# Optimization experiments

Hardware: AMD Instinct MI355X
Metric: run time of the kernel (lower is better)

The kernel has to match this reference:

```python
import jax, jax.numpy as jnp
import numpy as np

PAD_IDX = 0
NEG_INF = -1e30

N_USERS, N_ITEMS, N_SUBJECTS, EMB_DIM = 100000, 100000, 10000, 16
B, L = 16384, 50


def setup_inputs() -> dict:
    key = jax.random.key(0)
    ks = jax.random.split(key, 10)
    subj_emb = jax.random.normal(ks[0], (N_SUBJECTS, EMB_DIM), dtype=jnp.float32) * 0.1
    subj_emb = subj_emb.at[PAD_IDX].set(0.0)  # padding_idx row is zeros in torch
    attn_w = jax.random.normal(ks[1], (EMB_DIM,), dtype=jnp.float32) * 0.25
    attn_b = jnp.zeros((), dtype=jnp.float32)
    user_bias = jax.random.normal(ks[2], (N_USERS,), dtype=jnp.float32) * 0.05
    item_bias = jax.random.normal(ks[3], (N_ITEMS,), dtype=jnp.float32) * 0.05
    global_bias = jnp.zeros((), dtype=jnp.float32)
    user_idx = jax.random.randint(ks[4], (B,), 0, N_USERS)
    item_idx = jax.random.randint(ks[5], (B,), 0, N_ITEMS)
    fav_subjects = jax.random.randint(ks[6], (B, L), 0, N_SUBJECTS)
    book_subjects = jax.random.randint(ks[7], (B, L), 0, N_SUBJECTS)
    return {
        "subj_emb": subj_emb, "attn_w": attn_w, "attn_b": attn_b,
        "user_bias": user_bias, "item_bias": item_bias, "global_bias": global_bias,
        "user_idx": user_idx, "item_idx": item_idx,
        "fav_subjects": fav_subjects, "book_subjects": book_subjects,
    }


def attention_pool(indices, subj_emb, attn_w, attn_b):
    embs = subj_emb[indices]                      # [B, L, D] gather
    scores = embs @ attn_w + attn_b               # [B, L] tiny linear (D->1)
    mask = indices != PAD_IDX                     # [B, L]
    has_real = jnp.any(mask, axis=1)              # [B]
    # rows with no real subjects get position 0 unmasked (torch per-row loop)
    safe_mask = mask.at[:, 0].set(mask[:, 0] | ~has_real)
    scores = jnp.where(safe_mask, scores, NEG_INF)
    weights = jax.nn.softmax(scores, axis=1)      # [B, L]
    pooled = jnp.einsum("bld,bl->bd", embs, weights)
    return pooled  # dropout is identity in eval mode


def reference(subj_emb, attn_w, attn_b, user_bias, item_bias, global_bias,
              user_idx, item_idx, fav_subjects, book_subjects):
    u_emb = attention_pool(fav_subjects, subj_emb, attn_w, attn_b)   # [B, D]
    i_emb = attention_pool(book_subjects, subj_emb, attn_w, attn_b)  # [B, D]
    dot = jnp.sum(u_emb * i_emb, axis=1)                             # [B]
    return dot + user_bias[user_idx] + item_bias[item_idx] + global_bias
```

## Files before the change

### kernel.cpp

```cpp
#include <hip/hip_runtime.h>
#include <math.h>


#define PAD_IDX 0
constexpr int D = 16;
constexpr int ROWS_PER_BLOCK = 8;
constexpr int THREADS = 256;

template <int LFIX>
__global__ __launch_bounds__(256) void pool_kernel(
    const float* __restrict__ subj_emb,
    const float* __restrict__ attn_w,
    const float* __restrict__ attn_b,
    const float* __restrict__ user_bias,
    const float* __restrict__ item_bias,
    const float* __restrict__ global_bias,
    const int*  __restrict__ user_idx,
    const int*  __restrict__ item_idx,
    const int*  __restrict__ fav_subjects,
    const int*  __restrict__ book_subjects,
    float* __restrict__ out,
    int B)
{
    __shared__ int sidx[2][ROWS_PER_BLOCK * LFIX];

    const int row0  = blockIdx.x * ROWS_PER_BLOCK;
    const int nInts = ROWS_PER_BLOCK * LFIX;
    const long base = (long)row0 * LFIX;

    {
        const int n4 = nInts >> 2;
        const int4* fsrc = (const int4*)(fav_subjects  + base);
        const int4* bsrc = (const int4*)(book_subjects + base);
        int4* fdst = (int4*)sidx[0];
        int4* bdst = (int4*)sidx[1];
        for (int i = threadIdx.x; i < n4; i += THREADS) {
            fdst[i] = fsrc[i];
            bdst[i] = bsrc[i];
        }
        for (int i = (n4 << 2) + threadIdx.x; i < nInts; i += THREADS) {
            sidx[0][i] = fav_subjects[base + i];
            sidx[1][i] = book_subjects[base + i];
        }
    }
    __syncthreads();

    const int t    = threadIdx.x;
    const int r    = t >> 5;
    const int c    = (t >> 3) & 3;
    const int pool = (t >> 2) & 1;
    const int j    = t & 3;
    const int row  = row0 + r;

    const float4 wv = *(const float4*)(attn_w + 4 * j);
    const float  bb = attn_b[0];

    const int* __restrict__ idxl = sidx[pool] + r * LFIX;

    float4 acc = {0.f, 0.f, 0.f, 0.f};
    float  s   = 0.f;

    constexpr int ITERS = (LFIX + 3) / 4;
    #pragma unroll
    for (int k = 0; k < ITERS; ++k) {
        const int l  = c + 4 * k;
        const int si = (l < LFIX) ? idxl[l] : PAD_IDX;
        const float4 e = *(const float4*)(subj_emb + (long)si * D + 4 * j);
        float p = e.x * wv.x + e.y * wv.y + e.z * wv.z + e.w * wv.w;
        p += __shfl_xor(p, 1, 4);
        p += __shfl_xor(p, 2, 4);
        const float ew = __expf(p + bb);
        const float w  = (si != PAD_IDX) ? ew : 0.f;
        s     += w;
        acc.x += w * e.x;
        acc.y += w * e.y;
        acc.z += w * e.z;
        acc.w += w * e.w;
    }

    acc.x += __shfl_xor(acc.x, 8, 32);  acc.x += __shfl_xor(acc.x, 16, 32);
    acc.y += __shfl_xor(acc.y, 8, 32);  acc.y += __shfl_xor(acc.y, 16, 32);
    acc.z += __shfl_xor(acc.z, 8, 32);  acc.z += __shfl_xor(acc.z, 16, 32);
    acc.w += __shfl_xor(acc.w, 8, 32);  acc.w += __shfl_xor(acc.w, 16, 32);
    s     += __shfl_xor(s,     8, 32);  s     += __shfl_xor(s,     16, 32);

    const float inv = (s > 0.f) ? (1.f / s) : 0.f;
    float4 u;
    u.x = acc.x * inv; u.y = acc.y * inv; u.z = acc.z * inv; u.w = acc.w * inv;

    float4 o;
    o.x = __shfl_xor(u.x, 4, 8);
    o.y = __shfl_xor(u.y, 4, 8);
    o.z = __shfl_xor(u.z, 4, 8);
    o.w = __shfl_xor(u.w, 4, 8);

    float prod = u.x * o.x + u.y * o.y + u.z * o.z + u.w * o.w;
    prod += __shfl_xor(prod, 1, 4);
    prod += __shfl_xor(prod, 2, 4);

    if (row < B && (t & 31) == 0) {
        out[row] = prod + user_bias[user_idx[row]]
                        + item_bias[item_idx[row]]
                        + global_bias[0];
    }
}

__global__ __launch_bounds__(256) void pool_kernel_gen(
    const float* __restrict__ subj_emb,
    const float* __restrict__ attn_w,
    const float* __restrict__ attn_b,
    const float* __restrict__ user_bias,
    const float* __restrict__ item_bias,
    const float* __restrict__ global_bias,
    const int*  __restrict__ user_idx,
    const int*  __restrict__ item_idx,
    const int*  __restrict__ fav_subjects,
    const int*  __restrict__ book_subjects,
    float* __restrict__ out,
    int B, int L)
{
    __shared__ int sidx[2][ROWS_PER_BLOCK * 128];
    const int row0  = blockIdx.x * ROWS_PER_BLOCK;
    const int nInts = ROWS_PER_BLOCK * L;
    const long base = (long)row0 * L;
    for (int i = threadIdx.x; i < nInts; i += THREADS) {
        sidx[0][i] = fav_subjects[base + i];
        sidx[1][i] = book_subjects[base + i];
    }
    __syncthreads();

    const int t    = threadIdx.x;
    const int r    = t >> 5;
    const int c    = (t >> 3) & 3;
    const int pool = (t >> 2) & 1;
    const int j    = t & 3;
    const int row  = row0 + r;
    const float4 wv = *(const float4*)(attn_w + 4 * j);
    const float  bb = attn_b[0];
    const int* __restrict__ idxl = sidx[pool] + r * L;

    float4 acc = {0.f, 0.f, 0.f, 0.f};
    float  s   = 0.f;
    for (int l = c; l < L; l += 4) {
        const int si = idxl[l];
        const float4 e = *(const float4*)(subj_emb + (long)si * D + 4 * j);
        float p = e.x * wv.x + e.y * wv.y + e.z * wv.z + e.w * wv.w;
        p += __shfl_xor(p, 1, 4);
        p += __shfl_xor(p, 2, 4);
        const float ew = __expf(p + bb);
        const float w  = (si != PAD_IDX) ? ew : 0.f;
        s += w;
        acc.x += w * e.x; acc.y += w * e.y; acc.z += w * e.z; acc.w += w * e.w;
    }
    acc.x += __shfl_xor(acc.x, 8, 32);  acc.x += __shfl_xor(acc.x, 16, 32);
    acc.y += __shfl_xor(acc.y, 8, 32);  acc.y += __shfl_xor(acc.y, 16, 32);
    acc.z += __shfl_xor(acc.z, 8, 32);  acc.z += __shfl_xor(acc.z, 16, 32);
    acc.w += __shfl_xor(acc.w, 8, 32);  acc.w += __shfl_xor(acc.w, 16, 32);
    s     += __shfl_xor(s,     8, 32);  s     += __shfl_xor(s,     16, 32);
    const float inv = (s > 0.f) ? (1.f / s) : 0.f;
    float4 u = {acc.x * inv, acc.y * inv, acc.z * inv, acc.w * inv};
    float4 o;
    o.x = __shfl_xor(u.x, 4, 8); o.y = __shfl_xor(u.y, 4, 8);
    o.z = __shfl_xor(u.z, 4, 8); o.w = __shfl_xor(u.w, 4, 8);
    float prod = u.x * o.x + u.y * o.y + u.z * o.z + u.w * o.w;
    prod += __shfl_xor(prod, 1, 4);
    prod += __shfl_xor(prod, 2, 4);
    if (row < B && (t & 31) == 0) {
        out[row] = prod + user_bias[user_idx[row]]
                        + item_bias[item_idx[row]] + global_bias[0];
    }
}

extern "C" void kernel_launch(void* const* d_in, const int* in_sizes, int n_in,
                              void* d_out, int out_size, void* d_ws, size_t ws_size,
                              hipStream_t stream) {
    const float* subj_emb    = (const float*)d_in[0];
    const float* attn_w      = (const float*)d_in[1];
    const float* attn_b      = (const float*)d_in[2];
    const float* user_bias   = (const float*)d_in[3];
    const float* item_bias   = (const float*)d_in[4];
    const float* global_bias = (const float*)d_in[5];
    const int*   user_idx    = (const int*)d_in[6];
    const int*   item_idx    = (const int*)d_in[7];
    const int*   fav_subj    = (const int*)d_in[8];
    const int*   book_subj   = (const int*)d_in[9];
    float*       out         = (float*)d_out;

    const int D_ = 16;
    const int B  = in_sizes[6];
    const int L  = in_sizes[8] / B;
    (void)D_; (void)d_ws; (void)ws_size;

    const int blocks = (B + ROWS_PER_BLOCK - 1) / ROWS_PER_BLOCK;
    if (L == 50) {
        pool_kernel<50><<<blocks, THREADS, 0, stream>>>(
            subj_emb, attn_w, attn_b, user_bias, item_bias, global_bias,
            user_idx, item_idx, fav_subj, book_subj, out, B);
    } else {
        pool_kernel_gen<<<blocks, THREADS, 0, stream>>>(
            subj_emb, attn_w, attn_b, user_bias, item_bias, global_bias,
            user_idx, item_idx, fav_subj, book_subj, out, B, L);
    }
}
```

Measured before the change: 85.39 us.

## Use one wavefront per row and batch embedding gathers ahead of compute

Rows per block drop from 8 to 4, so each 64-lane wavefront handles one batch row with 8 positions in flight instead of 4. The index loads and all embedding gathers are issued before the softmax and accumulation loop, which raises memory-level parallelism and hides gather latency. The index copy to shared memory becomes a single predicated int4 load per thread. In exchange, more blocks are launched, more registers are held per thread for the preloaded embeddings, and the reductions now span the full wavefront.

```diff
diff --git a/kernel.cpp b/kernel.cpp
--- a/kernel.cpp
+++ b/kernel.cpp
@@ -4,7 +4,7 @@
 
 #define PAD_IDX 0
 constexpr int D = 16;
-constexpr int ROWS_PER_BLOCK = 8;
+constexpr int RPB = 4;
 constexpr int THREADS = 256;
 
 template <int LFIX>
@@ -15,74 +15,75 @@
     const float* __restrict__ user_bias,
     const float* __restrict__ item_bias,
     const float* __restrict__ global_bias,
+    const int*  __restrict__ fav_subjects,
+    const int*  __restrict__ book_subjects,
     const int*  __restrict__ user_idx,
     const int*  __restrict__ item_idx,
-    const int*  __restrict__ fav_subjects,
-    const int*  __restrict__ book_subjects,
     float* __restrict__ out,
     int B)
 {
-    __shared__ int sidx[2][ROWS_PER_BLOCK * LFIX];
-
-    const int row0  = blockIdx.x * ROWS_PER_BLOCK;
-    const int nInts = ROWS_PER_BLOCK * LFIX;
+    __shared__ int sidx[2][RPB * LFIX];
+
+    const int row0  = blockIdx.x * RPB;
     const long base = (long)row0 * LFIX;
 
     {
-        const int n4 = nInts >> 2;
+        constexpr int n4 = (RPB * LFIX) >> 2;
         const int4* fsrc = (const int4*)(fav_subjects  + base);
         const int4* bsrc = (const int4*)(book_subjects + base);
         int4* fdst = (int4*)sidx[0];
         int4* bdst = (int4*)sidx[1];
-        for (int i = threadIdx.x; i < n4; i += THREADS) {
-            fdst[i] = fsrc[i];
-            bdst[i] = bsrc[i];
-        }
-        for (int i = (n4 << 2) + threadIdx.x; i < nInts; i += THREADS) {
-            sidx[0][i] = fav_subjects[base + i];
-            sidx[1][i] = book_subjects[base + i];
-        }
+        const int t = threadIdx.x;
+        if (t < n4)            fdst[t]      = fsrc[t];
+        else if (t < 2 * n4)   bdst[t - n4] = bsrc[t - n4];
     }
     __syncthreads();
 
     const int t    = threadIdx.x;
-    const int r    = t >> 5;
-    const int c    = (t >> 3) & 3;
+    const int r    = t >> 6;
+    const int c    = (t >> 3) & 7;
     const int pool = (t >> 2) & 1;
     const int j    = t & 3;
     const int row  = row0 + r;
 
     const float4 wv = *(const float4*)(attn_w + 4 * j);
     const float  bb = attn_b[0];
-
     const int* __restrict__ idxl = sidx[pool] + r * LFIX;
+
+    constexpr int ITERS = (LFIX + 7) / 8;
+
+    int sis[ITERS];
+    #pragma unroll
+    for (int k = 0; k < ITERS; ++k) {
+        const int l = c + 8 * k;
+        sis[k] = (l < LFIX) ? idxl[l] : PAD_IDX;
+    }
+    float4 ev[ITERS];
+    #pragma unroll
+    for (int k = 0; k < ITERS; ++k)
+        ev[k] = *(const float4*)(subj_emb + (long)sis[k] * D + 4 * j);
 
     float4 acc = {0.f, 0.f, 0.f, 0.f};
     float  s   = 0.f;
-
-    constexpr int ITERS = (LFIX + 3) / 4;
     #pragma unroll
     for (int k = 0; k < ITERS; ++k) {
-        const int l  = c + 4 * k;
-        const int si = (l < LFIX) ? idxl[l] : PAD_IDX;
-        const float4 e = *(const float4*)(subj_emb + (long)si * D + 4 * j);
-        float p = e.x * wv.x + e.y * wv.y + e.z * wv.z + e.w * wv.w;
+        float p = ev[k].x * wv.x + ev[k].y * wv.y
+                + ev[k].z * wv.z + ev[k].w * wv.w;
         p += __shfl_xor(p, 1, 4);
         p += __shfl_xor(p, 2, 4);
-        const float ew = __expf(p + bb);
-        const float w  = (si != PAD_IDX) ? ew : 0.f;
+        const float w = (sis[k] != PAD_IDX) ? __expf(p + bb) : 0.f;
         s     += w;
-        acc.x += w * e.x;
-        acc.y += w * e.y;
-        acc.z += w * e.z;
-        acc.w += w * e.w;
-    }
-
-    acc.x += __shfl_xor(acc.x, 8, 32);  acc.x += __shfl_xor(acc.x, 16, 32);
-    acc.y += __shfl_xor(acc.y, 8, 32);  acc.y += __shfl_xor(acc.y, 16, 32);
-    acc.z += __shfl_xor(acc.z, 8, 32);  acc.z += __shfl_xor(acc.z, 16, 32);
-    acc.w += __shfl_xor(acc.w, 8, 32);  acc.w += __shfl_xor(acc.w, 16, 32);
-    s     += __shfl_xor(s,     8, 32);  s     += __shfl_xor(s,     16, 32);
+        acc.x += w * ev[k].x;
+        acc.y += w * ev[k].y;
+        acc.z += w * ev[k].z;
+        acc.w += w * ev[k].w;
+    }
+
+    acc.x += __shfl_xor(acc.x, 8, 64); acc.x += __shfl_xor(acc.x, 16, 64); acc.x += __shfl_xor(acc.x, 32, 64);
+    acc.y += __shfl_xor(acc.y, 8, 64); acc.y += __shfl_xor(acc.y, 16, 64); acc.y += __shfl_xor(acc.y, 32, 64);
+    acc.z += __shfl_xor(acc.z, 8, 64); acc.z += __shfl_xor(acc.z, 16, 64); acc.z += __shfl_xor(acc.z, 32, 64);
+    acc.w += __shfl_xor(acc.w, 8, 64); acc.w += __shfl_xor(acc.w, 16, 64); acc.w += __shfl_xor(acc.w, 32, 64);
+    s     += __shfl_xor(s,     8, 64); s     += __shfl_xor(s,     16, 64); s     += __shfl_xor(s,     32, 64);
 
     const float inv = (s > 0.f) ? (1.f / s) : 0.f;
     float4 u;
@@ -98,7 +99,7 @@
     prod += __shfl_xor(prod, 1, 4);
     prod += __shfl_xor(prod, 2, 4);
 
-    if (row < B && (t & 31) == 0) {
+    if (row < B && (t & 63) == 0) {
         out[row] = prod + user_bias[user_idx[row]]
                         + item_bias[item_idx[row]]
                         + global_bias[0];
@@ -112,16 +113,16 @@
     const float* __restrict__ user_bias,
     const float* __restrict__ item_bias,
     const float* __restrict__ global_bias,
+    const int*  __restrict__ fav_subjects,
+    const int*  __restrict__ book_subjects,
     const int*  __restrict__ user_idx,
     const int*  __restrict__ item_idx,
-    const int*  __restrict__ fav_subjects,
-    const int*  __restrict__ book_subjects,
     float* __restrict__ out,
     int B, int L)
 {
-    __shared__ int sidx[2][ROWS_PER_BLOCK * 128];
-    const int row0  = blockIdx.x * ROWS_PER_BLOCK;
-    const int nInts = ROWS_PER_BLOCK * L;
+    __shared__ int sidx[2][8 * 128];
+    const int row0  = blockIdx.x * 8;
+    const int nInts = 8 * L;
     const long base = (long)row0 * L;
     for (int i = threadIdx.x; i < nInts; i += THREADS) {
         sidx[0][i] = fav_subjects[base + i];
@@ -147,8 +148,7 @@
         float p = e.x * wv.x + e.y * wv.y + e.z * wv.z + e.w * wv.w;
         p += __shfl_xor(p, 1, 4);
         p += __shfl_xor(p, 2, 4);
-        const float ew = __expf(p + bb);
-        const float w  = (si != PAD_IDX) ? ew : 0.f;
+        const float w = (si != PAD_IDX) ? __expf(p + bb) : 0.f;
         s += w;
         acc.x += w * e.x; acc.y += w * e.y; acc.z += w * e.z; acc.w += w * e.w;
     }
@@ -185,20 +185,20 @@
     const int*   fav_subj    = (const int*)d_in[8];
     const int*   book_subj   = (const int*)d_in[9];
     float*       out         = (float*)d_out;
-
-    const int D_ = 16;
-    const int B  = in_sizes[6];
-    const int L  = in_sizes[8] / B;
-    (void)D_; (void)d_ws; (void)ws_size;
-
-    const int blocks = (B + ROWS_PER_BLOCK - 1) / ROWS_PER_BLOCK;
+    (void)d_ws; (void)ws_size;
+
+    const int B = in_sizes[6];
+    const int L = in_sizes[8] / B;
+
     if (L == 50) {
+        const int blocks = (B + RPB - 1) / RPB;
         pool_kernel<50><<<blocks, THREADS, 0, stream>>>(
             subj_emb, attn_w, attn_b, user_bias, item_bias, global_bias,
-            user_idx, item_idx, fav_subj, book_subj, out, B);
+            fav_subj, book_subj, user_idx, item_idx, out, B);
     } else {
+        const int blocks = (B + 7) / 8;
         pool_kernel_gen<<<blocks, THREADS, 0, stream>>>(
             subj_emb, attn_w, attn_b, user_bias, item_bias, global_bias,
-            user_idx, item_idx, fav_subj, book_subj, out, B, L);
+            fav_subj, book_subj, user_idx, item_idx, out, B, L);
     }
 }
```

New measurement: 85.55 us. About the same (+0.2%).
